# Performance work log

Hardware: AMD Instinct MI355X
Metric: run time of the kernel (lower is better)

Reference implementation:

```python
import jax, jax.numpy as jnp
import numpy as np
from jax.scipy.special import logsumexp

K = 15          # top-k
N = 4096        # n candidates
BS = 128        # batch size
EPS = 0.1       # entropic regularizer epsilon
MAX_ITER = 200  # Sinkhorn iterations
RANK = 5        # rank of pseudoinverse init
SMALL = 1e-20


def _build_weights():
    """Rank-5 pseudoinverse of Sinkhorn constraint matrix A (as in __init__).
    A maps (f in R^n, g in R^k) -> (f_i + g_c) over rows r = i*(k+1)+c (g_k := 0).
    A^T A = [[(k+1) I_n, J_{n x k}], [J_{k x n}, n I_k]] in closed form."""
    k1 = K + 1
    p = N + K
    G = np.zeros((p, p), dtype=np.float64)
    G[:N, :N] = (k1) * np.eye(N)
    G[:N, N:] = 1.0
    G[N:, :N] = 1.0
    G[N:, N:] = N * np.eye(K)
    w, V = np.linalg.eigh(G)
    idx = np.argsort(w)[-RANK:]
    s = np.sqrt(w[idx])
    V = V[:, idx]                                  # (p, RANK)
    # U = A @ V / s without materializing A (1GB dense):
    vf = V[:N]                                     # (N, RANK)
    vg = np.concatenate([V[N:], np.zeros((1, RANK))], axis=0)  # (k1, RANK)
    U = (vf[:, None, :] + vg[None, :, :]).reshape(N * k1, RANK) / s
    weight1 = (V / s).astype(np.float32)           # (N+K, RANK) = V diag(1/s)
    weight2 = U.T.astype(np.float32)               # (RANK, N*(K+1)) = U^T
    return jnp.asarray(weight1), jnp.asarray(weight2)


def setup_inputs() -> dict:
    key = jax.random.key(0)
    scores = jax.random.normal(key, (BS, N), dtype=jnp.float32)
    tau = jnp.ones((1,), jnp.float32) * 0.1
    weight1, weight2 = _build_weights()
    return {"scores": scores, "tau": tau, "weight1": weight1, "weight2": weight2}


def _sinkhorn(C, mu, nu, Gamma0, weight1, weight2):
    bs, n, k1 = C.shape
    # least-squares warm start for potentials f, g
    b = (C + EPS * jnp.log(Gamma0)).reshape(bs, -1)          # (bs, n*k1)
    x = jnp.einsum('bm,rm->br', b, weight2)                  # (bs, RANK)
    x = jnp.einsum('br,pr->bp', x, weight1)                  # (bs, n+k)
    f = x[:, :n, None]                                       # (bs, n, 1)
    g = jnp.concatenate([x[:, n:], jnp.zeros((bs, 1), C.dtype)], axis=-1)[:, None, :]  # (bs,1,k1)
    elog_mu = EPS * jnp.log(mu)                              # (1, n, 1)
    elog_nu = EPS * jnp.log(nu)                              # (1, 1, k1)

    def step(carry, _):
        f, g = carry
        f = -EPS * logsumexp(-(C - g) / EPS, axis=-1, keepdims=True) + elog_mu
        g = -EPS * logsumexp(-(C - f) / EPS, axis=-2, keepdims=True) + elog_nu
        return (f, g), None

    (f, g), _ = jax.lax.scan(step, (f, g), None, length=MAX_ITER)
    return jnp.exp((-C + f + g) / EPS)


def reference(scores, tau, weight1, weight2):
    bs, n = scores.shape
    k = K
    s = scores[:, :, None]                                   # (bs, n, 1)
    sd = jax.lax.stop_gradient(s)
    max_s = jnp.max(sd)
    min_s = jnp.min(jnp.where(jnp.isneginf(sd), jnp.inf, sd))
    filled = min_s - (max_s - min_s)
    s = jnp.where(jnp.isneginf(s), filled, s)
    anchors = jnp.arange(k, -1, -1, dtype=s.dtype).reshape(1, 1, k + 1)
    C = (s - anchors) ** 2
    C = C / jax.lax.stop_gradient(C.max())
    mu = jnp.full((1, n, 1), 1.0 / n, dtype=s.dtype)
    nu = jnp.concatenate([jnp.full((k,), 1.0 / n), jnp.array([(n - k) / n])]).astype(s.dtype).reshape(1, 1, k + 1)
    # warm-start transport plan Gamma0 from (detached) hard top-k
    topk_val = jax.lax.top_k(jax.lax.stop_gradient(s[..., 0]), k)[0]      # (bs, k)
    Gamma0 = jax.nn.sigmoid(-jnp.abs(topk_val[:, None, :] - s) / tau)     # (bs, n, k)
    Gamma0 = Gamma0 + SMALL
    Gamma0 = Gamma0 / Gamma0.sum(-2, keepdims=True) / n
    Gamma0_last = jnp.clip(1.0 / n - Gamma0.sum(-1, keepdims=True), SMALL, 1.0 - SMALL)
    Gamma0 = jnp.concatenate([Gamma0, Gamma0_last], axis=-1)              # (bs, n, k+1)
    Gamma = _sinkhorn(C, mu, nu, Gamma0, weight1, weight2)
    A = Gamma[:, :, :k] * n
    return A, jnp.linalg.norm(Gamma - Gamma0)
```

## Files before the change

kernel.cpp:

```cpp
#include <hip/hip_runtime.h>
#include <math.h>

#define KK 15
#define K1 16
#define NN 4096
#define BSZ 128
#define NT 512
#define RPT 8
#define NPAIR 4
#define NW 8
#define EPSI 0.1f
#define SMALLC 1e-20f
#define NITER 100
#define W2STRIDE 65536
#define OUT_A_ELEMS (BSZ * NN * KK)
#define TS 20
#define CONV_REL 2e-6f

typedef __attribute__((ext_vector_type(2))) float f2;
typedef __attribute__((ext_vector_type(2))) unsigned u2v;
__device__ __forceinline__ f2 pk_fma(f2 a, f2 b, f2 c){
  return __builtin_elementwise_fma(a, b, c);
}

__device__ __forceinline__ unsigned enc_f32(float f){
  unsigned u = __float_as_uint(f);
  return (u & 0x80000000u) ? ~u : (u | 0x80000000u);
}
__device__ __forceinline__ float dec_f32(unsigned e){
  unsigned u = (e & 0x80000000u) ? (e ^ 0x80000000u) : ~e;
  return __uint_as_float(u);
}


template<int CTRL>
__device__ __forceinline__ float dpp_movf(float x){
  return __uint_as_float((unsigned)__builtin_amdgcn_update_dpp(
      (int)0, (int)__float_as_uint(x), CTRL, 0xF, 0xF, true));
}

__device__ __forceinline__ float bcast_lane0(float x){
  return __uint_as_float((unsigned)__builtin_amdgcn_readlane(
      (int)__float_as_uint(x), 0));
}

__device__ __forceinline__ float xsum16(float r){
#if __has_builtin(__builtin_amdgcn_permlane16_swap)
  u2v s = __builtin_amdgcn_permlane16_swap(__float_as_uint(r), __float_as_uint(r), false, false);
  return __uint_as_float(s.x) + __uint_as_float(s.y);
#else
  return r + __shfl_xor(r, 16);
#endif
}
__device__ __forceinline__ float xsum32(float r){
#if __has_builtin(__builtin_amdgcn_permlane32_swap)
  u2v s = __builtin_amdgcn_permlane32_swap(__float_as_uint(r), __float_as_uint(r), false, false);
  return __uint_as_float(s.x) + __uint_as_float(s.y);
#else
  return r + __shfl_xor(r, 32);
#endif
}

__device__ __forceinline__ float sum16_all(float v){
  v += dpp_movf<0x128>(v);
  v += dpp_movf<0x124>(v);
  v += dpp_movf<0x4E>(v);
  v += dpp_movf<0xB1>(v);
  return v;
}

__device__ __forceinline__ int fold_col(int lane){
  int l = lane & 15;
  return ((l & 1) << 3) | ((l & 2) << 1) | ((l & 8) >> 2) | ((l & 4) >> 2);
}

__device__ __forceinline__ float wave_fold16(const float p[K1], int lane){
  float a[8];
  {
    const bool hi = (lane & 1) != 0;
    #pragma unroll
    for (int j = 0; j < 8; ++j){
      float send = hi ? p[j] : p[j + 8];
      float keep = hi ? p[j + 8] : p[j];
      a[j] = keep + dpp_movf<0xB1>(send);
    }
  }
  float bq[4];
  {
    const bool hi = (lane & 2) != 0;
    #pragma unroll
    for (int j = 0; j < 4; ++j){
      float send = hi ? a[j] : a[j + 4];
      float keep = hi ? a[j + 4] : a[j];
      bq[j] = keep + dpp_movf<0x4E>(send);
    }
  }
  float cq[2];
  {
    const bool hi = (lane & 8) != 0;
    float s0 = hi ? bq[0] : bq[2];
    float s1 = hi ? bq[1] : bq[3];
    float k0 = hi ? bq[2] : bq[0];
    float k1 = hi ? bq[3] : bq[1];
    cq[0] = k0 + dpp_movf<0x128>(s0);
    cq[1] = k1 + dpp_movf<0x128>(s1);
  }
  float r;
  {
    const bool hi = (lane & 4) != 0;
    float send = hi ? cq[0] : cq[1];
    float keep = hi ? cq[1] : cq[0];
    r = keep + __shfl_xor(send, 4);
  }
  r = xsum16(r);
  r = xsum32(r);
  return r;
}

__device__ __forceinline__ void block_fold16(const float p[K1], float* wb, float* tb,
                                             int lane, int wv, int tid){
  float r = wave_fold16(p, lane);
  if (lane < 16) wb[wv * K1 + fold_col(lane)] = r;
  __syncthreads();
  if (tid < 16){
    float t = 0.0f;
    #pragma unroll
    for (int q = 0; q < NW; ++q) t += wb[q * K1 + tid];
    tb[tid] = t;
  }
  __syncthreads();
}

__global__ __launch_bounds__(NT, 2) void k_main(
    const float* __restrict__ scores, const float* __restrict__ taup,
    const float* __restrict__ w1, const float* __restrict__ w2,
    float* __restrict__ out, unsigned* __restrict__ ws){
  const int b = blockIdx.x;
  const int tid = threadIdx.x;
  const int lane = tid & 63;
  const int wv = tid >> 6;

  __shared__ float tk[KK];
  __shared__ float cands[NW * KK];
  __shared__ __align__(16) float cbuf[K1];
  __shared__ float wbuf[NW * K1];
  __shared__ __align__(16) float xbuf[K1];
  __shared__ __align__(16) float wbufT[2][K1 * TS];
  __shared__ float rv[NW];
  __shared__ float rmn[NW];
  __shared__ unsigned sng[NW];
  __shared__ float statb[4];

  float raw[RPT];
  #pragma unroll
  for (int j = 0; j < RPT; ++j) raw[j] = scores[(size_t)b * NN + tid + NT * j];

  {
    float mx = -INFINITY, mn = INFINITY; unsigned neg = 0u;
    #pragma unroll
    for (int j = 0; j < RPT; ++j){
      float v = raw[j];
      mx = fmaxf(mx, v);
      if (v == -INFINITY) neg = 1u; else mn = fminf(mn, v);
    }
    #pragma unroll
    for (int off = 32; off; off >>= 1){
      mx = fmaxf(mx, __shfl_xor(mx, off));
      mn = fminf(mn, __shfl_xor(mn, off));
      neg |= (unsigned)__shfl_xor((int)neg, off);
    }
    if (lane == 0){ rv[wv] = mx; rmn[wv] = mn; sng[wv] = neg; }
    __syncthreads();
    if (tid == 0){
      for (int q = 1; q < NW; ++q){
        mx = fmaxf(mx, rv[q]); mn = fminf(mn, rmn[q]); neg |= sng[q];
      }
      atomicMax(&ws[0], enc_f32(mx));
      atomicMin(&ws[5], enc_f32(mn));
      if (neg) atomicOr(&ws[1], 1u);
      __threadfence();
      atomicAdd(&ws[3], 1u);
      while (__hip_atomic_load(&ws[3], __ATOMIC_ACQUIRE, __HIP_MEMORY_SCOPE_AGENT) < (unsigned)BSZ)
        __builtin_amdgcn_s_sleep(2);
      statb[0] = dec_f32(__hip_atomic_load(&ws[0], __ATOMIC_RELAXED, __HIP_MEMORY_SCOPE_AGENT));
      statb[1] = dec_f32(__hip_atomic_load(&ws[5], __ATOMIC_RELAXED, __HIP_MEMORY_SCOPE_AGENT));
      statb[2] = __hip_atomic_load(&ws[1], __ATOMIC_RELAXED, __HIP_MEMORY_SCOPE_AGENT) ? 1.0f : 0.0f;
    }
    __syncthreads();
  }

  const float smax = statb[0];
  const float smin_raw = statb[1];
  const bool has_neg = statb[2] != 0.0f;
  const float filled = smin_raw - (smax - smin_raw);
  const float smin_eff = has_neg ? filled : smin_raw;
  const float cmax = fmaxf(fmaxf(smin_eff * smin_eff, smax * smax),
                           fmaxf((smin_eff - 15.0f) * (smin_eff - 15.0f),
                                 (smax - 15.0f) * (smax - 15.0f)));
  const float cinv = 1.0f / cmax;
  const float tauv = taup[0];
  const float invtau = 1.0f / tauv;
  const float inv_n = 1.0f / (float)NN;

  float sv[RPT];
  #pragma unroll
  for (int j = 0; j < RPT; ++j){
    float v = raw[j]; if (v == -INFINITY) v = filled;
    sv[j] = v;
  }

  {
    float lv[RPT];
    #pragma unroll
    for (int j = 0; j < RPT; ++j) lv[j] = sv[j];
    #pragma unroll
    for (int t = 0; t < KK; ++t){
      float bv = lv[0]; int bs = 0;
      #pragma unroll
      for (int j = 1; j < RPT; ++j){ if (lv[j] > bv){ bv = lv[j]; bs = j; } }
      int bidx = (lane << 3) | bs;
      #pragma unroll
      for (int off = 32; off; off >>= 1){
        float ov = __shfl_xor(bv, off);
        int oi = __shfl_xor(bidx, off);
        if (ov > bv || (ov == bv && oi < bidx)){ bv = ov; bidx = oi; }
      }
      if ((bidx >> 3) == lane){
        int s = bidx & 7;
        #pragma unroll
        for (int j = 0; j < RPT; ++j) if (j == s) lv[j] = -INFINITY;
      }
      if (lane == 0) cands[wv * KK + t] = bv;
    }
  }
  __syncthreads();
  if (wv == 0){
    float c0 = (lane < NW * KK) ? cands[lane] : -INFINITY;
    float c1 = (lane + 64 < NW * KK) ? cands[lane + 64] : -INFINITY;
    #pragma unroll
    for (int t = 0; t < KK; ++t){
      int sel = (c0 >= c1) ? 0 : 1;
      float bv = sel ? c1 : c0;
      int bidx = (lane << 1) | sel;
      #pragma unroll
      for (int off = 32; off; off >>= 1){
        float ov = __shfl_xor(bv, off);
        int oi = __shfl_xor(bidx, off);
        if (ov > bv || (ov == bv && oi < bidx)){ bv = ov; bidx = oi; }
      }
      if ((bidx >> 1) == lane){
        if ((bidx & 1) == 0) c0 = -INFINITY; else c1 = -INFINITY;
      }
      if (lane == 0) tk[t] = bv;
    }
  }
  __syncthreads();

  {
    float p[K1];
    float tkr[KK];
    #pragma unroll
    for (int c = 0; c < KK; ++c) tkr[c] = tk[c];
    #pragma unroll
    for (int c = 0; c < K1; ++c) p[c] = 0.0f;
    #pragma unroll
    for (int j = 0; j < RPT; ++j){
      float si = sv[j];
      #pragma unroll
      for (int c = 0; c < KK; ++c){
        float z = fabsf(tkr[c] - si) * invtau;
        float raw1 = __builtin_amdgcn_rcpf(1.0f + __expf(z)) + SMALLC;
        p[c] += raw1;
      }
    }
    block_fold16(p, wbuf, cbuf, lane, wv, tid);
  }

  float colinv_n[KK];
  {
    float p[K1];
    float tkr[KK];
    #pragma unroll
    for (int c = 0; c < KK; ++c){
      tkr[c] = tk[c];
      colinv_n[c] = (1.0f / cbuf[c]) * inv_n;
    }
    #pragma unroll
    for (int c = 0; c < K1; ++c) p[c] = 0.0f;
    #pragma unroll
    for (int j = 0; j < RPT; ++j){
      int i = tid + NT * j;
      float si = sv[j];
      float bb[K1];
      float rowpart = 0.0f;
      #pragma unroll
      for (int c = 0; c < KK; ++c){
        float d = si - (float)(KK - c);
        float Cc = d * d * cinv;
        float z = fabsf(tkr[c] - si) * invtau;
        float raw1 = __builtin_amdgcn_rcpf(1.0f + __expf(z)) + SMALLC;
        float g0 = raw1 * colinv_n[c];
        rowpart += g0;
        bb[c] = Cc + EPSI * __logf(g0);
      }
      {
        float Cc = si * si * cinv;
        float g0l = fminf(fmaxf(inv_n - rowpart, SMALLC), 1.0f - SMALLC);
        bb[KK] = Cc + EPSI * __logf(g0l);
      }
      #pragma unroll
      for (int r = 0; r < 5; ++r){
        const float4* wp = (const float4*)(w2 + (size_t)r * W2STRIDE + (size_t)i * K1);
        float4 a0 = wp[0], a1 = wp[1], a2 = wp[2], a3 = wp[3];
        float acc = p[r];
        acc += bb[0] * a0.x + bb[1] * a0.y + bb[2] * a0.z + bb[3] * a0.w;
        acc += bb[4] * a1.x + bb[5] * a1.y + bb[6] * a1.z + bb[7] * a1.w;
        acc += bb[8] * a2.x + bb[9] * a2.y + bb[10] * a2.z + bb[11] * a2.w;
        acc += bb[12] * a3.x + bb[13] * a3.y + bb[14] * a3.z + bb[15] * a3.w;
        p[r] = acc;
      }
    }
    block_fold16(p, wbuf, xbuf, lane, wv, tid);
  }

  float vt[K1];
  {
    float xv[5];
    #pragma unroll
    for (int r = 0; r < 5; ++r) xv[r] = xbuf[r];
    #pragma unroll
    for (int c = 0; c < KK; ++c){
      float g = 0.0f;
      #pragma unroll
      for (int r = 0; r < 5; ++r) g += xv[r] * w1[(size_t)(NN + c) * 5 + r];
      float Bc = expf(-10.0f * cinv * (float)((KK - c) * (KK - c)));
      vt[c] = Bc * expf(g * 10.0f);
    }
    vt[KK] = 1.0f;
  }

  f2 x2[NPAIR];
  #pragma unroll
  for (int q = 0; q < NPAIR; ++q){
    x2[q].x = expf(sv[2 * q] * (-20.0f * cinv));
    x2[q].y = expf(sv[2 * q + 1] * (-20.0f * cinv));
  }
  f2 xp[NPAIR][K1];
  #pragma unroll
  for (int q = 0; q < NPAIR; ++q){
    xp[q][0].x = 1.0f; xp[q][0].y = 1.0f;
    xp[q][1] = x2[q];
    #pragma unroll
    for (int c = 2; c < K1; ++c) xp[q][c] = xp[q][c - 1] * x2[q];
  }

  f2 t2[NPAIR];
  const float nmul = ((lane & 15) < KK) ? 1.0f : 4081.0f;
  float pv2 = 0.0f, pv1 = 0.0f;
  int pcnt = -1;
  #pragma unroll 1
  for (int it = 0; it < NITER; ++it){
    const int ph = it & 1;
    #pragma unroll
    for (int q = 0; q < NPAIR; ++q){
      f2 h; h.x = vt[KK]; h.y = vt[KK];
      #pragma unroll
      for (int c = KK - 1; c >= 0; --c){
        f2 vc; vc.x = vt[c]; vc.y = vt[c];
        h = pk_fma(h, x2[q], vc);
      }
      t2[q].x = __builtin_amdgcn_rcpf(h.x);
      t2[q].y = __builtin_amdgcn_rcpf(h.y);
    }
    float p[K1];
    #pragma unroll
    for (int c = 0; c < K1; ++c){
      f2 s = t2[0] * xp[0][c];
      #pragma unroll
      for (int q = 1; q < NPAIR; ++q) s = pk_fma(t2[q], xp[q][c], s);
      p[c] = s.x + s.y;
    }
    float r = wave_fold16(p, lane);
    if (lane < 16) wbufT[ph][fold_col(lane) * TS + wv] = r;
    __syncthreads();
    float md = -1.0f;
    float wout = 0.0f;
    if (lane < 16){
      const float* wp = &wbufT[ph][lane * TS];
      float4 a4 = *(const float4*)wp;
      float4 b4 = *(const float4*)(wp + 4);
      float t = ((a4.x + a4.y) + (a4.z + a4.w)) + ((b4.x + b4.y) + (b4.z + b4.w));
      float wnew = nmul * __builtin_amdgcn_rcpf(t);
      md = fabsf(wnew - pv1) - CONV_REL * pv1;
      wout = wnew;
    }
    if (pcnt >= 1){
      float r1 = 0.0f, r2 = 0.0f;
      if (lane < 16){
        float winv = __builtin_amdgcn_rcpf(wout);
        r1 = (pv1 - pv2) * winv;
        r2 = (wout - pv1) * winv;
      }
      float s12 = sum16_all(r1 * r2);
      float s11 = sum16_all(r1 * r1);
      float s12b = bcast_lane0(s12);
      float s11b = bcast_lane0(s11);
      int anymove = __any((lane < 16) && (fabsf(r2) > 4.0f * CONV_REL));
      float fac = s12b * __builtin_amdgcn_rcpf(s11b - s12b);
      float acc = wout * (1.0f + r2 * fac);
      int okbr = (lane < 16) ? (acc > 0.1f * wout && acc < 10.0f * wout) : 1;
      int allbr = __all(okbr);
      if ((s12b > 0.0f) && (s12b < 0.97f * s11b) && anymove && allbr){
        if (lane < 16) wout = acc;
        pcnt = -1;
      }
    }
    pcnt++;
    pv2 = pv1; pv1 = wout;
    int conv = __all(md <= 0.0f);
    #pragma unroll
    for (int c = 0; c < K1; ++c)
      vt[c] = __uint_as_float((unsigned)__builtin_amdgcn_readlane(
                  (int)__float_as_uint(wout), c));
    if (conv) break;
  }

  float nrm = 0.0f;
  {
    float tkr[KK];
    #pragma unroll
    for (int c = 0; c < KK; ++c) tkr[c] = tk[c];
    #pragma unroll
    for (int q = 0; q < NPAIR; ++q){
      #pragma unroll
      for (int half = 0; half < 2; ++half){
        int i = tid + NT * (2 * q + half);
        float si = sv[2 * q + half];
        float tin = (half ? t2[q].y : t2[q].x) * inv_n;
        float rowpart = 0.0f;
        float gamv[KK];
        float gaml;
        #pragma unroll
        for (int c = 0; c < KK; ++c){
          float xc = half ? xp[q][c].y : xp[q][c].x;
          float gam = (tin * xc) * vt[c];
          float z = fabsf(tkr[c] - si) * invtau;
          float raw1 = __builtin_amdgcn_rcpf(1.0f + __expf(z)) + SMALLC;
          float g0 = raw1 * colinv_n[c];
          rowpart += g0;
          float d = gam - g0;
          nrm += d * d;
          gamv[c] = gam * (float)NN;
        }
        {
          float xc = half ? xp[q][KK].y : xp[q][KK].x;
          gaml = (tin * xc) * vt[KK];
          float g0l = fminf(fmaxf(inv_n - rowpart, SMALLC), 1.0f - SMALLC);
          float d = gaml - g0l;
          nrm += d * d;
        }
        float* op = out + (size_t)(b * NN + i) * KK;
        #pragma unroll
        for (int c = 0; c < KK; ++c) op[c] = gamv[c];
      }
    }
  }
  #pragma unroll
  for (int off = 32; off; off >>= 1) nrm += __shfl_xor(nrm, off);
  if (lane == 0) rv[wv] = nrm;
  __syncthreads();
  if (tid == 0){
    float t = 0.0f;
    for (int q = 0; q < NW; ++q) t += rv[q];
    atomicAdd(reinterpret_cast<float*>(ws) + 2, t);
    __threadfence();
    unsigned prev = atomicAdd(&ws[4], 1u);
    if (prev == (unsigned)(BSZ - 1)){
      float n2 = __hip_atomic_load(reinterpret_cast<float*>(ws) + 2,
                                   __ATOMIC_RELAXED, __HIP_MEMORY_SCOPE_AGENT);
      out[OUT_A_ELEMS] = sqrtf(n2);
    }
  }
}

extern "C" void kernel_launch(void* const* d_in, const int* in_sizes, int n_in,
                              void* d_out, int out_size, void* d_ws, size_t ws_size,
                              hipStream_t stream){
  const float* scores = (const float*)d_in[0];
  const float* tau    = (const float*)d_in[1];
  const float* w1     = (const float*)d_in[2];
  const float* w2     = (const float*)d_in[3];
  float* out = (float*)d_out;
  unsigned* ws = (unsigned*)d_ws;

  hipMemsetAsync(ws, 0x00, 20, stream);
  hipMemsetAsync((char*)ws + 20, 0xFF, 4, stream);

  k_main<<<BSZ, NT, 0, stream>>>(scores, tau, w1, w2, out, ws);
}
```

Before: 152.0 us.

## Factor warm-start projection through weight1, fix Sinkhorn iterations, merge memsets

The warm-start projection no longer streams the large weight2 matrix (5 x 65536 floats per batch). It uses the structure U = A V / s, so each row's contribution becomes its row-sum times weight1[i] plus column sums times the g-part of weight1. The Sinkhorn loop drops its convergence test and runs a fixed 52 iterations, with extrapolation disabled in the last two. The min-reduction slot is encoded with a bitwise complement so one zero memset replaces two memsets. The fixed iteration count may do more or fewer iterations than the old adaptive exit, and convergence quality now rests on that count.

```diff
diff --git a/kernel.cpp b/kernel.cpp
--- a/kernel.cpp
+++ b/kernel.cpp
@@ -11,11 +11,10 @@
 #define NW 8
 #define EPSI 0.1f
 #define SMALLC 1e-20f
-#define NITER 100
+#define NITER 52
 #define W2STRIDE 65536
 #define OUT_A_ELEMS (BSZ * NN * KK)
 #define TS 20
-#define CONV_REL 2e-6f
 
 typedef __attribute__((ext_vector_type(2))) float f2;
 typedef __attribute__((ext_vector_type(2))) unsigned u2v;
@@ -145,6 +144,8 @@
   __shared__ __align__(16) float cbuf[K1];
   __shared__ float wbuf[NW * K1];
   __shared__ __align__(16) float xbuf[K1];
+  __shared__ __align__(16) float bbcol[K1];
+  __shared__ float xv5[8];
   __shared__ __align__(16) float wbufT[2][K1 * TS];
   __shared__ float rv[NW];
   __shared__ float rmn[NW];
@@ -176,14 +177,14 @@
         mx = fmaxf(mx, rv[q]); mn = fminf(mn, rmn[q]); neg |= sng[q];
       }
       atomicMax(&ws[0], enc_f32(mx));
-      atomicMin(&ws[5], enc_f32(mn));
+      atomicMax(&ws[5], ~enc_f32(mn));
       if (neg) atomicOr(&ws[1], 1u);
       __threadfence();
       atomicAdd(&ws[3], 1u);
       while (__hip_atomic_load(&ws[3], __ATOMIC_ACQUIRE, __HIP_MEMORY_SCOPE_AGENT) < (unsigned)BSZ)
         __builtin_amdgcn_s_sleep(2);
       statb[0] = dec_f32(__hip_atomic_load(&ws[0], __ATOMIC_RELAXED, __HIP_MEMORY_SCOPE_AGENT));
-      statb[1] = dec_f32(__hip_atomic_load(&ws[5], __ATOMIC_RELAXED, __HIP_MEMORY_SCOPE_AGENT));
+      statb[1] = dec_f32(~__hip_atomic_load(&ws[5], __ATOMIC_RELAXED, __HIP_MEMORY_SCOPE_AGENT));
       statb[2] = __hip_atomic_load(&ws[1], __ATOMIC_RELAXED, __HIP_MEMORY_SCOPE_AGENT) ? 1.0f : 0.0f;
     }
     __syncthreads();
@@ -278,7 +279,8 @@
 
   float colinv_n[KK];
   {
-    float p[K1];
+    float pcol[K1];
+    float prow[K1];
     float tkr[KK];
     #pragma unroll
     for (int c = 0; c < KK; ++c){
@@ -286,7 +288,7 @@
       colinv_n[c] = (1.0f / cbuf[c]) * inv_n;
     }
     #pragma unroll
-    for (int c = 0; c < K1; ++c) p[c] = 0.0f;
+    for (int c = 0; c < K1; ++c){ pcol[c] = 0.0f; prow[c] = 0.0f; }
     #pragma unroll
     for (int j = 0; j < RPT; ++j){
       int i = tid + NT * j;
@@ -308,26 +310,35 @@
         float g0l = fminf(fmaxf(inv_n - rowpart, SMALLC), 1.0f - SMALLC);
         bb[KK] = Cc + EPSI * __logf(g0l);
       }
-      #pragma unroll
-      for (int r = 0; r < 5; ++r){
-        const float4* wp = (const float4*)(w2 + (size_t)r * W2STRIDE + (size_t)i * K1);
-        float4 a0 = wp[0], a1 = wp[1], a2 = wp[2], a3 = wp[3];
-        float acc = p[r];
-        acc += bb[0] * a0.x + bb[1] * a0.y + bb[2] * a0.z + bb[3] * a0.w;
-        acc += bb[4] * a1.x + bb[5] * a1.y + bb[6] * a1.z + bb[7] * a1.w;
-        acc += bb[8] * a2.x + bb[9] * a2.y + bb[10] * a2.z + bb[11] * a2.w;
-        acc += bb[12] * a3.x + bb[13] * a3.y + bb[14] * a3.z + bb[15] * a3.w;
-        p[r] = acc;
-      }
-    }
-    block_fold16(p, wbuf, xbuf, lane, wv, tid);
+      float rs = 0.0f;
+      #pragma unroll
+      for (int c = 0; c < K1; ++c){ pcol[c] += bb[c]; rs += bb[c]; }
+      const float* w1r = w1 + (size_t)i * 5;
+      float4 wA = *(const float4*)w1r;
+      float w4 = w1r[4];
+      prow[0] = fmaf(wA.x, rs, prow[0]);
+      prow[1] = fmaf(wA.y, rs, prow[1]);
+      prow[2] = fmaf(wA.z, rs, prow[2]);
+      prow[3] = fmaf(wA.w, rs, prow[3]);
+      prow[4] = fmaf(w4,  rs, prow[4]);
+    }
+    block_fold16(pcol, wbuf, bbcol, lane, wv, tid);
+    block_fold16(prow, wbuf, xbuf, lane, wv, tid);
+    if (tid < 5){
+      float xr = xbuf[tid];
+      #pragma unroll
+      for (int c = 0; c < KK; ++c)
+        xr = fmaf(w1[(size_t)(NN + c) * 5 + tid], bbcol[c], xr);
+      xv5[tid] = xr;
+    }
+    __syncthreads();
   }
 
   float vt[K1];
   {
     float xv[5];
     #pragma unroll
-    for (int r = 0; r < 5; ++r) xv[r] = xbuf[r];
+    for (int r = 0; r < 5; ++r) xv[r] = xv5[r];
     #pragma unroll
     for (int c = 0; c < KK; ++c){
       float g = 0.0f;
@@ -383,18 +394,15 @@
     float r = wave_fold16(p, lane);
     if (lane < 16) wbufT[ph][fold_col(lane) * TS + wv] = r;
     __syncthreads();
-    float md = -1.0f;
     float wout = 0.0f;
     if (lane < 16){
       const float* wp = &wbufT[ph][lane * TS];
       float4 a4 = *(const float4*)wp;
       float4 b4 = *(const float4*)(wp + 4);
       float t = ((a4.x + a4.y) + (a4.z + a4.w)) + ((b4.x + b4.y) + (b4.z + b4.w));
-      float wnew = nmul * __builtin_amdgcn_rcpf(t);
-      md = fabsf(wnew - pv1) - CONV_REL * pv1;
-      wout = wnew;
-    }
-    if (pcnt >= 1){
+      wout = nmul * __builtin_amdgcn_rcpf(t);
+    }
+    if (pcnt >= 1 && it < NITER - 2){
       float r1 = 0.0f, r2 = 0.0f;
       if (lane < 16){
         float winv = __builtin_amdgcn_rcpf(wout);
@@ -405,24 +413,21 @@
       float s11 = sum16_all(r1 * r1);
       float s12b = bcast_lane0(s12);
       float s11b = bcast_lane0(s11);
-      int anymove = __any((lane < 16) && (fabsf(r2) > 4.0f * CONV_REL));
       float fac = s12b * __builtin_amdgcn_rcpf(s11b - s12b);
       float acc = wout * (1.0f + r2 * fac);
       int okbr = (lane < 16) ? (acc > 0.1f * wout && acc < 10.0f * wout) : 1;
       int allbr = __all(okbr);
-      if ((s12b > 0.0f) && (s12b < 0.97f * s11b) && anymove && allbr){
+      if ((s12b > 0.0f) && (s12b < 0.97f * s11b) && allbr){
         if (lane < 16) wout = acc;
         pcnt = -1;
       }
     }
     pcnt++;
     pv2 = pv1; pv1 = wout;
-    int conv = __all(md <= 0.0f);
     #pragma unroll
     for (int c = 0; c < K1; ++c)
       vt[c] = __uint_as_float((unsigned)__builtin_amdgcn_readlane(
                   (int)__float_as_uint(wout), c));
-    if (conv) break;
   }
 
   float nrm = 0.0f;
@@ -493,8 +498,7 @@
   float* out = (float*)d_out;
   unsigned* ws = (unsigned*)d_ws;
 
-  hipMemsetAsync(ws, 0x00, 20, stream);
-  hipMemsetAsync((char*)ws + 20, 0xFF, 4, stream);
+  hipMemsetAsync(ws, 0x00, 24, stream);
 
   k_main<<<BSZ, NT, 0, stream>>>(scores, tau, w1, w2, out, ws);
 }
```

New measurement: 239.7 us. 1.58x slower.
